# Kernel tuning notes

Hardware: AMD Instinct MI355X
Metric: run time of the kernel (lower is better)

Reference implementation:

```python
import jax, jax.numpy as jnp
import numpy as np

B, SQ, SK, D = 16, 2048, 2048, 64


def setup_inputs() -> dict:
    key = jax.random.key(0)
    kq, kk, kv, kl = jax.random.split(key, 4)
    queries = jax.random.normal(kq, (B, SQ, D), dtype=jnp.float32)
    keys = jax.random.normal(kk, (B, SK, D), dtype=jnp.float32)
    values = jax.random.normal(kv, (B, SK, D), dtype=jnp.float32)
    # per-batch valid key lengths in [1, SK]
    valid_lens = jax.random.randint(kl, (B,), 1, SK + 1)
    return {"queries": queries, "keys": keys, "values": values, "valid_lens": valid_lens}


def reference(queries, keys, values, valid_lens):
    d = queries.shape[-1]
    # scaled scores: [B, SQ, SK]
    scores = jnp.einsum('bqd,bkd->bqk', queries, keys) / jnp.sqrt(jnp.asarray(d, queries.dtype))
    # masked_softmax (d2l): positions >= valid_len get -1e6 before softmax
    key_pos = jnp.arange(scores.shape[-1])  # [SK]
    mask = key_pos[None, None, :] < valid_lens[:, None, None]  # [B,1,SK]
    scores = jnp.where(mask, scores, jnp.asarray(-1e6, scores.dtype))
    attn = jax.nn.softmax(scores, axis=-1)
    # dropout p=0.0 -> identity
    return jnp.einsum('bqk,bkd->bqd', attn, values)
```

## Files before the change

### kernel.cpp

```cpp
#include <hip/hip_runtime.h>

#define NB  16
#define SQn 2048
#define SKn 2048
#define DHn 64

typedef float    f32x4 __attribute__((ext_vector_type(4)));
typedef _Float16 f16x8 __attribute__((ext_vector_type(8)));
typedef _Float16 f16x4 __attribute__((ext_vector_type(4)));

#define MFMA __builtin_amdgcn_mfma_f32_16x16x32_f16

__device__ __forceinline__ f16x8 cvt8(f32x4 a, f32x4 b) {
    f16x8 h;
    h[0] = (_Float16)a[0]; h[1] = (_Float16)a[1];
    h[2] = (_Float16)a[2]; h[3] = (_Float16)a[3];
    h[4] = (_Float16)b[0]; h[5] = (_Float16)b[1];
    h[6] = (_Float16)b[2]; h[7] = (_Float16)b[3];
    return h;
}

#ifndef USE_GLDS
#define USE_GLDS 1
#endif

__device__ __forceinline__ void stage16(const void* g, unsigned char* base, int lane) {
#if USE_GLDS
    __builtin_amdgcn_global_load_lds(
        (const __attribute__((address_space(1))) unsigned int*)g,
        (__attribute__((address_space(3))) unsigned int*)base,
        16, 0, 0);
#else
    *(f16x8*)(base + lane * 16) = *(const f16x8*)g;
#endif
}

__global__ __launch_bounds__(256)
void prep_kernel(const float* __restrict__ Kg, const float* __restrict__ Vg,
                 _Float16* __restrict__ Kh, _Float16* __restrict__ VTh)
{
    const int tid = threadIdx.x;
    const int kt  = blockIdx.x;
    const int b   = blockIdx.y;
    const size_t tbase = ((size_t)b * SKn + (size_t)kt * 64) * DHn;

    {
        const float* s = Kg + tbase + tid * 16;
        f32x4 a0 = *(const f32x4*)(s);
        f32x4 a1 = *(const f32x4*)(s + 4);
        f32x4 a2 = *(const f32x4*)(s + 8);
        f32x4 a3 = *(const f32x4*)(s + 12);
        _Float16* d = Kh + tbase + tid * 16;
        *(f16x8*)d       = cvt8(a0, a1);
        *(f16x8*)(d + 8) = cvt8(a2, a3);
    }
    __shared__ float vt[64][68];
    {
        const int row = tid >> 2, cb = (tid & 3) * 16;
        const float* s = Vg + tbase + row * DHn + cb;
#pragma unroll
        for (int i = 0; i < 4; ++i)
            *(f32x4*)&vt[row][cb + 4 * i] = *(const f32x4*)(s + 4 * i);
    }
    __syncthreads();
    {
        const int d0 = tid >> 2, kc = (tid & 3) * 16;
        f16x8 o0, o1;
#pragma unroll
        for (int j = 0; j < 8; ++j) {
            o0[j] = (_Float16)vt[kc + j][d0];
            o1[j] = (_Float16)vt[kc + 8 + j][d0];
        }
        _Float16* d = VTh + ((size_t)b * DHn + d0) * SKn + (size_t)kt * 64 + kc;
        *(f16x8*)d       = o0;
        *(f16x8*)(d + 8) = o1;
    }
}

__global__ __launch_bounds__(256, 2)
void attn_fwd2(const float* __restrict__ Qg, const _Float16* __restrict__ Kh,
               const _Float16* __restrict__ VTh, const int* __restrict__ VL,
               float* __restrict__ Og)
{
    const int tid   = threadIdx.x;
    const int wave  = tid >> 6;
    const int lane  = tid & 63;
    const int l15   = lane & 15;
    const int q4    = lane >> 4;
    const int qhalf = wave & 1;
    const int kpar  = wave >> 1;

    const int b  = blockIdx.x & 15;
    const int qb = blockIdx.x >> 4;

    __shared__ __align__(16) unsigned char smem[49152];
    unsigned char* Kt0 = smem;
    unsigned char* Kt1 = smem + 8192;
    unsigned char* Vt0 = smem + 16384;
    unsigned char* Vt1 = smem + 24576;
    unsigned char* Pb  = smem + 32768 + wave * 4096;
    float* mergeO = (float*)smem;
    float* mergeL = (float*)(smem + 32768);

    const int vl      = VL[b];
    const int ntiles  = (vl + 63) >> 6;
    const int nrounds = (ntiles + 1) >> 1;

    const float SCALE = 0.18033688011112042f;
    const int qbase = qb * 64 + qhalf * 32;

    f16x8 qf[2][2];
#pragma unroll
    for (int g = 0; g < 2; ++g) {
        const float* qrow = Qg + ((size_t)b * SQn + qbase + g * 16 + l15) * DHn + q4 * 8;
#pragma unroll
        for (int c = 0; c < 2; ++c) {
            f32x4 a  = *(const f32x4*)(qrow + c * 32);
            f32x4 a2 = *(const f32x4*)(qrow + c * 32 + 4);
            a *= SCALE; a2 *= SCALE;
            qf[g][c] = cvt8(a, a2);
        }
    }

    f32x4 O[2][4];
#pragma unroll
    for (int g = 0; g < 2; ++g)
#pragma unroll
        for (int t = 0; t < 4; ++t) O[g][t] = (f32x4){0.f, 0.f, 0.f, 0.f};
    float lacc[2] = {0.f, 0.f};

    const _Float16* KhB = Kh + (size_t)b * SKn * DHn;
    const _Float16* VTB = VTh + (size_t)b * DHn * SKn;

    const int slot0 = tid;
    const int slot1 = 256 + tid;
    const int row0 = slot0 >> 3, gl0 = (slot0 & 7) ^ (row0 & 7);
    const int row1 = slot1 >> 3, gl1 = (slot1 & 7) ^ (row1 & 7);
    const int lbase0 = (0 * 256 + wave * 64) * 16;
    const int lbase1 = (1 * 256 + wave * 64) * 16;

    for (int r = 0; r < nrounds; ++r) {
        {
            const int ka = 2 * r * 64, kb = (2 * r + 1) * 64;
            stage16(KhB + (size_t)(ka + row0) * DHn + gl0 * 8, Kt0 + lbase0, lane);
            stage16(KhB + (size_t)(ka + row1) * DHn + gl1 * 8, Kt0 + lbase1, lane);
            stage16(KhB + (size_t)(kb + row0) * DHn + gl0 * 8, Kt1 + lbase0, lane);
            stage16(KhB + (size_t)(kb + row1) * DHn + gl1 * 8, Kt1 + lbase1, lane);
            stage16(VTB + (size_t)row0 * SKn + ka + gl0 * 8, Vt0 + lbase0, lane);
            stage16(VTB + (size_t)row1 * SKn + ka + gl1 * 8, Vt0 + lbase1, lane);
            stage16(VTB + (size_t)row0 * SKn + kb + gl0 * 8, Vt1 + lbase0, lane);
            stage16(VTB + (size_t)row1 * SKn + kb + gl1 * 8, Vt1 + lbase1, lane);
        }
        __syncthreads();

        const int kt = 2 * r + kpar;
        if (kt < ntiles) {
            const unsigned char* Kb = kpar ? Kt1 : Kt0;
            const unsigned char* Vb = kpar ? Vt1 : Vt0;
            const int sw = l15 & 7;

            f32x4 st[2][4];
#pragma unroll
            for (int g = 0; g < 2; ++g)
#pragma unroll
                for (int t = 0; t < 4; ++t) st[g][t] = (f32x4){0.f, 0.f, 0.f, 0.f};
#pragma unroll
            for (int t = 0; t < 4; ++t) {
                const int row = 16 * t + l15;
#pragma unroll
                for (int c = 0; c < 2; ++c) {
                    f16x8 kf = *(const f16x8*)(Kb + row * 128 + ((((c << 2) | q4) ^ sw) * 16));
                    st[0][t] = MFMA(kf, qf[0][c], st[0][t], 0, 0, 0);
                    st[1][t] = MFMA(kf, qf[1][c], st[1][t], 0, 0, 0);
                }
            }

            const bool lastt = (kt == ntiles - 1) && (vl & 63);
#pragma unroll
            for (int g = 0; g < 2; ++g) {
                unsigned char* pdst = Pb + (g * 16 + l15) * 128 + (q4 & 1) * 8;
#pragma unroll
                for (int t = 0; t < 4; ++t) {
                    float p0 = __builtin_amdgcn_exp2f(st[g][t][0]);
                    float p1 = __builtin_amdgcn_exp2f(st[g][t][1]);
                    float p2 = __builtin_amdgcn_exp2f(st[g][t][2]);
                    float p3 = __builtin_amdgcn_exp2f(st[g][t][3]);
                    if (lastt) {
                        const int kb0 = kt * 64 + 16 * t + 4 * q4;
                        p0 = (kb0 + 0 < vl) ? p0 : 0.f;
                        p1 = (kb0 + 1 < vl) ? p1 : 0.f;
                        p2 = (kb0 + 2 < vl) ? p2 : 0.f;
                        p3 = (kb0 + 3 < vl) ? p3 : 0.f;
                    }
                    lacc[g] += (p0 + p1) + (p2 + p3);
                    f16x4 w;
                    w[0] = (_Float16)p0; w[1] = (_Float16)p1;
                    w[2] = (_Float16)p2; w[3] = (_Float16)p3;
                    *(f16x4*)(pdst + (((2 * t + (q4 >> 1)) ^ sw) * 16)) = w;
                }
            }
            asm volatile("" ::: "memory");

            f16x8 pf[2][2];
#pragma unroll
            for (int g = 0; g < 2; ++g) {
                const unsigned char* psrc = Pb + (g * 16 + l15) * 128;
                pf[g][0] = *(const f16x8*)(psrc + ((q4 ^ sw) * 16));
                pf[g][1] = *(const f16x8*)(psrc + (((4 | q4) ^ sw) * 16));
            }

#pragma unroll
            for (int t2 = 0; t2 < 4; ++t2) {
                const int row = 16 * t2 + l15;
#pragma unroll
                for (int c2 = 0; c2 < 2; ++c2) {
                    f16x8 vf = *(const f16x8*)(Vb + row * 128 + ((((c2 << 2) | q4) ^ sw) * 16));
                    O[0][t2] = MFMA(vf, pf[0][c2], O[0][t2], 0, 0, 0);
                    O[1][t2] = MFMA(vf, pf[1][c2], O[1][t2], 0, 0, 0);
                }
            }
        }
        __syncthreads();
    }

    if (kpar == 1) {
#pragma unroll
        for (int g = 0; g < 2; ++g) {
            const int x = g * 16 + l15;
#pragma unroll
            for (int t2 = 0; t2 < 4; ++t2) {
                const int gd = (4 * t2 + q4) ^ l15;
                *(f32x4*)((unsigned char*)mergeO + (qhalf * 32 + x) * 256 + gd * 16) = O[g][t2];
            }
            float lt = lacc[g];
            lt += __shfl_xor(lt, 16);
            lt += __shfl_xor(lt, 32);
            if (q4 == 0) mergeL[qhalf * 32 + x] = lt;
        }
    }
    __syncthreads();
    if (kpar == 0) {
#pragma unroll
        for (int g = 0; g < 2; ++g) {
            const int x = g * 16 + l15;
            float lt = lacc[g];
            lt += __shfl_xor(lt, 16);
            lt += __shfl_xor(lt, 32);
            lt += mergeL[qhalf * 32 + x];
            const float inv = 1.f / lt;
            float* orow = Og + ((size_t)b * SQn + qbase + x) * DHn;
#pragma unroll
            for (int t2 = 0; t2 < 4; ++t2) {
                const int gd = (4 * t2 + q4) ^ l15;
                f32x4 part = *(const f32x4*)((const unsigned char*)mergeO + (qhalf * 32 + x) * 256 + gd * 16);
                f32x4 res = (O[g][t2] + part) * inv;
                *(f32x4*)(orow + 16 * t2 + 4 * q4) = res;
            }
        }
    }
}

__global__ __launch_bounds__(256, 2)
void attn_fwd(const float* __restrict__ Qg, const float* __restrict__ Kg,
              const float* __restrict__ Vg, const int* __restrict__ VL,
              float* __restrict__ Og)
{
    const int tid  = threadIdx.x;
    const int wave = tid >> 6;
    const int lane = tid & 63;
    const int l15  = lane & 15;
    const int q4   = lane >> 4;
    const int b  = blockIdx.x & 15;
    const int qb = blockIdx.x >> 4;
    __shared__ __align__(16) unsigned char smemf[8192 + 8192 + 4 * 2048];
    unsigned char* Klds  = smemf;
    unsigned char* VTlds = smemf + 8192;
    unsigned char* Plds  = smemf + 16384 + wave * 2048;
    const int vl = VL[b];
    const int ntiles = (vl + 63) >> 6;
    const float SCALE = 0.18033688011112042f;
    f16x8 qfr[2];
    {
        const float* qrow = Qg + ((size_t)b * SQn + (size_t)qb * 64 + wave * 16 + l15) * DHn;
#pragma unroll
        for (int c = 0; c < 2; ++c) {
            const float* s = qrow + c * 32 + q4 * 8;
            f32x4 a = *(const f32x4*)s;
            f32x4 b2 = *(const f32x4*)(s + 4);
            a *= SCALE; b2 *= SCALE;
            qfr[c] = cvt8(a, b2);
        }
    }
    f32x4 O[4];
#pragma unroll
    for (int t = 0; t < 4; ++t) O[t] = (f32x4){0.f, 0.f, 0.f, 0.f};
    float m_i[4] = {-3e38f, -3e38f, -3e38f, -3e38f};
    float l_i[4] = {0.f, 0.f, 0.f, 0.f};
    for (int kt = 0; kt < ntiles; ++kt) {
        const int k0 = kt * 64;
#pragma unroll
        for (int i = 0; i < 2; ++i) {
            int g8 = tid + i * 256;
            int row = g8 >> 3, g = g8 & 7;
            const float* s = Kg + ((size_t)b * SKn + k0 + row) * DHn + g * 8;
            f32x4 a = *(const f32x4*)s;
            f32x4 c4 = *(const f32x4*)(s + 4);
            *(f16x8*)(Klds + row * 128 + ((g ^ (row & 7)) * 16)) = cvt8(a, c4);
        }
        {
            int key = tid & 63, dg = tid >> 6;
            const float* s = Vg + ((size_t)b * SKn + k0 + key) * DHn + dg * 16;
            int swz = key >> 3;
            int koff = (key & 7) * 2;
#pragma unroll
            for (int i = 0; i < 4; ++i) {
                f32x4 v4 = *(const f32x4*)(s + i * 4);
#pragma unroll
                for (int j = 0; j < 4; ++j) {
                    int d = dg * 16 + i * 4 + j;
                    *(_Float16*)(VTlds + d * 128 + ((swz ^ (d & 7)) * 16) + koff) = (_Float16)v4[j];
                }
            }
        }
        __syncthreads();
        f32x4 accs[4];
#pragma unroll
        for (int t = 0; t < 4; ++t) accs[t] = (f32x4){0.f, 0.f, 0.f, 0.f};
#pragma unroll
        for (int t = 0; t < 4; ++t) {
            int row = t * 16 + l15;
#pragma unroll
            for (int c = 0; c < 2; ++c) {
                f16x8 kf = *(const f16x8*)(Klds + row * 128 + ((((c << 2) + q4) ^ (l15 & 7)) * 16));
                accs[t] = MFMA(qfr[c], kf, accs[t], 0, 0, 0);
            }
        }
        if (k0 + 64 > vl) {
#pragma unroll
            for (int t = 0; t < 4; ++t)
                if (k0 + t * 16 + l15 >= vl) accs[t] = (f32x4){-1e30f, -1e30f, -1e30f, -1e30f};
        }
        float al[4];
#pragma unroll
        for (int rr = 0; rr < 4; ++rr) {
            float v = fmaxf(fmaxf(accs[0][rr], accs[1][rr]), fmaxf(accs[2][rr], accs[3][rr]));
            v = fmaxf(v, __shfl_xor(v, 1));
            v = fmaxf(v, __shfl_xor(v, 2));
            v = fmaxf(v, __shfl_xor(v, 4));
            v = fmaxf(v, __shfl_xor(v, 8));
            float mnew = fmaxf(m_i[rr], v);
            al[rr] = __builtin_amdgcn_exp2f(m_i[rr] - mnew);
            m_i[rr] = mnew;
        }
#pragma unroll
        for (int rr = 0; rr < 4; ++rr) {
            float s0 = 0.f;
#pragma unroll
            for (int t = 0; t < 4; ++t) {
                float p = __builtin_amdgcn_exp2f(accs[t][rr] - m_i[rr]);
                accs[t][rr] = p;
                s0 += p;
            }
            s0 += __shfl_xor(s0, 1);
            s0 += __shfl_xor(s0, 2);
            s0 += __shfl_xor(s0, 4);
            s0 += __shfl_xor(s0, 8);
            l_i[rr] = l_i[rr] * al[rr] + s0;
            O[0][rr] *= al[rr]; O[1][rr] *= al[rr]; O[2][rr] *= al[rr]; O[3][rr] *= al[rr];
        }
#pragma unroll
        for (int rr = 0; rr < 4; ++rr) {
            int row = q4 * 4 + rr;
            int swz = row & 7;
#pragma unroll
            for (int t = 0; t < 4; ++t) {
                int g = t * 2 + (l15 >> 3);
                *(_Float16*)(Plds + row * 128 + ((g ^ swz) * 16) + (l15 & 7) * 2) = (_Float16)accs[t][rr];
            }
        }
        asm volatile("" ::: "memory");
        f16x8 pfr[2];
        pfr[0] = *(const f16x8*)(Plds + l15 * 128 + ((q4 ^ (l15 & 7)) * 16));
        pfr[1] = *(const f16x8*)(Plds + l15 * 128 + (((4 + q4) ^ (l15 & 7)) * 16));
#pragma unroll
        for (int t2 = 0; t2 < 4; ++t2) {
            int d = t2 * 16 + l15;
#pragma unroll
            for (int c2 = 0; c2 < 2; ++c2) {
                f16x8 vf = *(const f16x8*)(VTlds + d * 128 + ((((c2 << 2) + q4) ^ (l15 & 7)) * 16));
                O[t2] = MFMA(pfr[c2], vf, O[t2], 0, 0, 0);
            }
        }
        __syncthreads();
    }
    float inv[4];
#pragma unroll
    for (int rr = 0; rr < 4; ++rr) inv[rr] = 1.f / l_i[rr];
    float* orow = Og + ((size_t)b * SQn + (size_t)qb * 64 + wave * 16 + q4 * 4) * DHn;
#pragma unroll
    for (int rr = 0; rr < 4; ++rr)
#pragma unroll
        for (int t2 = 0; t2 < 4; ++t2)
            orow[rr * DHn + t2 * 16 + l15] = O[t2][rr] * inv[rr];
}

extern "C" void kernel_launch(void* const* d_in, const int* in_sizes, int n_in,
                              void* d_out, int out_size, void* d_ws, size_t ws_size,
                              hipStream_t stream) {
    (void)in_sizes; (void)n_in; (void)out_size;
    const float* Q = (const float*)d_in[0];
    const float* K = (const float*)d_in[1];
    const float* V = (const float*)d_in[2];
    const int*  VLp = (const int*)d_in[3];
    float* O = (float*)d_out;

    const size_t elems = (size_t)NB * SKn * DHn;
    const size_t need  = elems * 2 * sizeof(_Float16);
    if (ws_size >= need) {
        _Float16* Kh  = (_Float16*)d_ws;
        _Float16* VTh = Kh + elems;
        hipLaunchKernelGGL(prep_kernel, dim3(SKn / 64, NB), dim3(256), 0, stream, K, V, Kh, VTh);
        hipLaunchKernelGGL(attn_fwd2, dim3(NB * (SQn / 64)), dim3(256), 0, stream, Q, Kh, VTh, VLp, O);
    } else {
        hipLaunchKernelGGL(attn_fwd, dim3(NB * (SQn / 64)), dim3(256), 0, stream, Q, K, V, VLp, O);
    }
}
```

Baseline: 100.5 us.

## Split key range across four blocks per query tile and add merge kernel

The attention kernel now splits each batch's key tiles across KS=4 independent blocks, interleaved with stride 8 tiles. Each block writes unnormalized partial outputs and row sums to workspace, and a new merge kernel sums them and normalizes. The aim is better load balance and more blocks when per-batch valid lengths vary, since previously the longest batch bounded the single-wave grid. In exchange it adds workspace traffic for the partial outputs and an extra kernel launch. It also raises the workspace requirement, and if that is not met the code falls back to the old path.

Result: slower. 117.5 us (+17.0%).

```diff
diff --git a/kernel.cpp b/kernel.cpp
--- a/kernel.cpp
+++ b/kernel.cpp
@@ -4,6 +4,7 @@
 #define SQn 2048
 #define SKn 2048
 #define DHn 64
+#define KS  4
 
 typedef float    f32x4 __attribute__((ext_vector_type(4)));
 typedef _Float16 f16x8 __attribute__((ext_vector_type(8)));
@@ -20,19 +21,11 @@
     return h;
 }
 
-#ifndef USE_GLDS
-#define USE_GLDS 1
-#endif
-
-__device__ __forceinline__ void stage16(const void* g, unsigned char* base, int lane) {
-#if USE_GLDS
+__device__ __forceinline__ void stage16(const void* g, unsigned char* base) {
     __builtin_amdgcn_global_load_lds(
         (const __attribute__((address_space(1))) unsigned int*)g,
         (__attribute__((address_space(3))) unsigned int*)base,
         16, 0, 0);
-#else
-    *(f16x8*)(base + lane * 16) = *(const f16x8*)g;
-#endif
 }
 
 __global__ __launch_bounds__(256)
@@ -77,10 +70,10 @@
     }
 }
 
-__global__ __launch_bounds__(256, 2)
-void attn_fwd2(const float* __restrict__ Qg, const _Float16* __restrict__ Kh,
-               const _Float16* __restrict__ VTh, const int* __restrict__ VL,
-               float* __restrict__ Og)
+__global__ __launch_bounds__(256)
+void attn_split(const float* __restrict__ Qg, const _Float16* __restrict__ Kh,
+                const _Float16* __restrict__ VTh, const int* __restrict__ VL,
+                float* __restrict__ Opart, float* __restrict__ lpart)
 {
     const int tid   = threadIdx.x;
     const int wave  = tid >> 6;
@@ -91,7 +84,13 @@
     const int kpar  = wave >> 1;
 
     const int b  = blockIdx.x & 15;
-    const int qb = blockIdx.x >> 4;
+    const int qb = (blockIdx.x >> 4) & 31;
+    const int ks = blockIdx.x >> 9;
+
+    const int vl     = VL[b];
+    const int ntiles = (vl + 63) >> 6;
+    if (ntiles <= ks) return;
+    const int nrounds = ((ntiles - ks - 1) >> 3) + 1;
 
     __shared__ __align__(16) unsigned char smem[49152];
     unsigned char* Kt0 = smem;
@@ -102,10 +101,6 @@
     float* mergeO = (float*)smem;
     float* mergeL = (float*)(smem + 32768);
 
-    const int vl      = VL[b];
-    const int ntiles  = (vl + 63) >> 6;
-    const int nrounds = (ntiles + 1) >> 1;
-
     const float SCALE = 0.18033688011112042f;
     const int qbase = qb * 64 + qhalf * 32;
 
@@ -132,28 +127,29 @@
     const _Float16* KhB = Kh + (size_t)b * SKn * DHn;
     const _Float16* VTB = VTh + (size_t)b * DHn * SKn;
 
-    const int slot0 = tid;
-    const int slot1 = 256 + tid;
+    const int slot0 = tid, slot1 = 256 + tid;
     const int row0 = slot0 >> 3, gl0 = (slot0 & 7) ^ (row0 & 7);
     const int row1 = slot1 >> 3, gl1 = (slot1 & 7) ^ (row1 & 7);
-    const int lbase0 = (0 * 256 + wave * 64) * 16;
-    const int lbase1 = (1 * 256 + wave * 64) * 16;
+    const int lbase0 = (wave * 64) * 16;
+    const int lbase1 = (256 + wave * 64) * 16;
 
     for (int r = 0; r < nrounds; ++r) {
+        const int tileA = ks + 8 * r;
+        const int tileB = tileA + 4;
         {
-            const int ka = 2 * r * 64, kb = (2 * r + 1) * 64;
-            stage16(KhB + (size_t)(ka + row0) * DHn + gl0 * 8, Kt0 + lbase0, lane);
-            stage16(KhB + (size_t)(ka + row1) * DHn + gl1 * 8, Kt0 + lbase1, lane);
-            stage16(KhB + (size_t)(kb + row0) * DHn + gl0 * 8, Kt1 + lbase0, lane);
-            stage16(KhB + (size_t)(kb + row1) * DHn + gl1 * 8, Kt1 + lbase1, lane);
-            stage16(VTB + (size_t)row0 * SKn + ka + gl0 * 8, Vt0 + lbase0, lane);
-            stage16(VTB + (size_t)row1 * SKn + ka + gl1 * 8, Vt0 + lbase1, lane);
-            stage16(VTB + (size_t)row0 * SKn + kb + gl0 * 8, Vt1 + lbase0, lane);
-            stage16(VTB + (size_t)row1 * SKn + kb + gl1 * 8, Vt1 + lbase1, lane);
+            const int ka = tileA * 64, kb = tileB * 64;
+            stage16(KhB + (size_t)(ka + row0) * DHn + gl0 * 8, Kt0 + lbase0);
+            stage16(KhB + (size_t)(ka + row1) * DHn + gl1 * 8, Kt0 + lbase1);
+            stage16(KhB + (size_t)(kb + row0) * DHn + gl0 * 8, Kt1 + lbase0);
+            stage16(KhB + (size_t)(kb + row1) * DHn + gl1 * 8, Kt1 + lbase1);
+            stage16(VTB + (size_t)row0 * SKn + ka + gl0 * 8, Vt0 + lbase0);
+            stage16(VTB + (size_t)row1 * SKn + ka + gl1 * 8, Vt0 + lbase1);
+            stage16(VTB + (size_t)row0 * SKn + kb + gl0 * 8, Vt1 + lbase0);
+            stage16(VTB + (size_t)row1 * SKn + kb + gl1 * 8, Vt1 + lbase1);
         }
         __syncthreads();
 
-        const int kt = 2 * r + kpar;
+        const int kt = kpar ? tileB : tileA;
         if (kt < ntiles) {
             const unsigned char* Kb = kpar ? Kt1 : Kt0;
             const unsigned char* Vb = kpar ? Vt1 : Vt0;
@@ -240,6 +236,7 @@
     }
     __syncthreads();
     if (kpar == 0) {
+        const size_t rowbase = (size_t)b * SQn + qbase;
 #pragma unroll
         for (int g = 0; g < 2; ++g) {
             const int x = g * 16 + l15;
@@ -247,17 +244,39 @@
             lt += __shfl_xor(lt, 16);
             lt += __shfl_xor(lt, 32);
             lt += mergeL[qhalf * 32 + x];
-            const float inv = 1.f / lt;
-            float* orow = Og + ((size_t)b * SQn + qbase + x) * DHn;
+            if (q4 == 0) lpart[(size_t)ks * (NB * SQn) + rowbase + x] = lt;
+            float* orow = Opart + ((size_t)ks * (NB * SQn) + rowbase + x) * DHn;
 #pragma unroll
             for (int t2 = 0; t2 < 4; ++t2) {
                 const int gd = (4 * t2 + q4) ^ l15;
                 f32x4 part = *(const f32x4*)((const unsigned char*)mergeO + (qhalf * 32 + x) * 256 + gd * 16);
-                f32x4 res = (O[g][t2] + part) * inv;
-                *(f32x4*)(orow + 16 * t2 + 4 * q4) = res;
-            }
-        }
-    }
+                *(f32x4*)(orow + 16 * t2 + 4 * q4) = O[g][t2] + part;
+            }
+        }
+    }
+}
+
+__global__ __launch_bounds__(256)
+void merge_kernel(const float* __restrict__ Op, const float* __restrict__ lp,
+                  const int* __restrict__ VL, float* __restrict__ Og)
+{
+    const int i   = blockIdx.x * 256 + threadIdx.x;
+    const int row = i >> 4;
+    const int dc  = (i & 15) * 4;
+    const int b   = row >> 11;
+    const int ntiles = (VL[b] + 63) >> 6;
+    const int nact   = ntiles < KS ? ntiles : KS;
+
+    f32x4 acc = (f32x4){0.f, 0.f, 0.f, 0.f};
+    float l = 0.f;
+    for (int s = 0; s < nact; ++s) {
+        acc += *(const f32x4*)(Op + ((size_t)s * (NB * SQn) + row) * DHn + dc);
+        l   += lp[(size_t)s * (NB * SQn) + row];
+    }
+    const float inv = 1.f / l;
+    f32x4 r = acc;
+    r *= inv;
+    *(f32x4*)(Og + (size_t)row * DHn + dc) = r;
 }
 
 __global__ __launch_bounds__(256, 2)
@@ -414,13 +433,24 @@
     const int*  VLp = (const int*)d_in[3];
     float* O = (float*)d_out;
 
-    const size_t elems = (size_t)NB * SKn * DHn;
-    const size_t need  = elems * 2 * sizeof(_Float16);
+    const size_t kv_elems = (size_t)NB * SKn * DHn;
+    const size_t rows     = (size_t)NB * SQn;
+    const size_t off_Kh = 0;
+    const size_t off_VT = kv_elems * sizeof(_Float16);
+    const size_t off_Op = off_VT + kv_elems * sizeof(_Float16);
+    const size_t off_lp = off_Op + (size_t)KS * rows * DHn * sizeof(float);
+    const size_t need   = off_lp + (size_t)KS * rows * sizeof(float);
+
     if (ws_size >= need) {
-        _Float16* Kh  = (_Float16*)d_ws;
-        _Float16* VTh = Kh + elems;
+        _Float16* Kh  = (_Float16*)((char*)d_ws + off_Kh);
+        _Float16* VTh = (_Float16*)((char*)d_ws + off_VT);
+        float* Opart  = (float*)((char*)d_ws + off_Op);
+        float* lpart  = (float*)((char*)d_ws + off_lp);
         hipLaunchKernelGGL(prep_kernel, dim3(SKn / 64, NB), dim3(256), 0, stream, K, V, Kh, VTh);
-        hipLaunchKernelGGL(attn_fwd2, dim3(NB * (SQn / 64)), dim3(256), 0, stream, Q, Kh, VTh, VLp, O);
+        hipLaunchKernelGGL(attn_split, dim3(NB * (SQn / 64) * KS), dim3(256), 0, stream,
+                           Q, Kh, VTh, VLp, Opart, lpart);
+        hipLaunchKernelGGL(merge_kernel, dim3((NB * SQn * DHn / 4) / 256), dim3(256), 0, stream,
+                           Opart, lpart, VLp, O);
     } else {
         hipLaunchKernelGGL(attn_fwd, dim3(NB * (SQn / 64)), dim3(256), 0, stream, Q, K, V, VLp, O);
     }
```
